# Kernel tuning notes

Hardware: AMD Instinct MI355X
Metric: run time of the kernel (lower is better)

Reference implementation:

```python
import jax, jax.numpy as jnp
import numpy as np

B, NA, LD, AD = 2048, 8, 256, 256
D = LD + AD            # token_dim = 512
E, K, H = 4, 2, 8      # n_experts, top_k, n_attention_heads
FFN, HEAD, BINS = 2048, 512, 101
DH = D // H
LN_EPS = 1e-5


def setup_inputs() -> dict:
    key = jax.random.key(0)
    ks = jax.random.split(key, 9)
    s = 0.02
    return {
        "latents": jax.random.normal(ks[0], (B, NA, LD), jnp.float32),
        "actions": jax.random.normal(ks[1], (B, NA, AD), jnp.float32),
        "gate_W": jax.random.normal(ks[2], (NA * D, E), jnp.float32) * s,
        "Wqkv": jax.random.normal(ks[3], (E, D, 3 * D), jnp.float32) * s,
        "bqkv": jnp.zeros((E, 3 * D), jnp.float32),
        "Wo": jax.random.normal(ks[4], (E, D, D), jnp.float32) * s,
        "bo": jnp.zeros((E, D), jnp.float32),
        "ln1_g": jnp.ones((E, D), jnp.float32),
        "ln1_b": jnp.zeros((E, D), jnp.float32),
        "Wf1": jax.random.normal(ks[5], (E, D, FFN), jnp.float32) * s,
        "bf1": jnp.zeros((E, FFN), jnp.float32),
        "Wf2": jax.random.normal(ks[6], (E, FFN, D), jnp.float32) * s,
        "bf2": jnp.zeros((E, D), jnp.float32),
        "ln2_g": jnp.ones((E, D), jnp.float32),
        "ln2_b": jnp.zeros((E, D), jnp.float32),
        "head_W1": jax.random.normal(ks[7], (NA * D, HEAD), jnp.float32) * s,
        "head_b1": jnp.zeros((HEAD,), jnp.float32),
        "head_W2": jax.random.normal(ks[8], (HEAD, BINS), jnp.float32) * s,
        "head_b2": jnp.zeros((BINS,), jnp.float32),
    }


def _layernorm(x, g, b):
    mu = x.mean(-1, keepdims=True)
    var = ((x - mu) ** 2).mean(-1, keepdims=True)
    return (x - mu) / jnp.sqrt(var + LN_EPS) * g + b


def _expert(tokens, Wqkv, bqkv, Wo, bo, g1, b1, Wf1, bf1, Wf2, bf2, g2, b2):
    # tokens: [B, N, D] -> self-attention + FFN block (pre-residual, post-LN)
    b, n, d = tokens.shape
    qkv = tokens @ Wqkv + bqkv                                  # [B, N, 3D]
    q, k, v = jnp.split(qkv, 3, axis=-1)
    heads = lambda x: x.reshape(b, n, H, DH).transpose(0, 2, 1, 3)  # [B, H, N, dh]
    q, k, v = heads(q), heads(k), heads(v)
    scores = jnp.einsum("bhqd,bhkd->bhqk", q, k) / np.float32(np.sqrt(DH))
    attn = jax.nn.softmax(scores, axis=-1)
    ctx = jnp.einsum("bhqk,bhkd->bhqd", attn, v).transpose(0, 2, 1, 3).reshape(b, n, d)
    x = _layernorm(tokens + ctx @ Wo + bo, g1, b1)
    h = jax.nn.relu(x @ Wf1 + bf1) @ Wf2 + bf2
    return _layernorm(x + h, g2, b2)


def _cv2(x):
    # coefficient of variation squared (unbiased var, matches torch .var())
    x = x.astype(jnp.float32)
    return jnp.var(x, ddof=1) / (jnp.mean(x) ** 2 + 1e-10)


def reference(latents, actions, gate_W, Wqkv, bqkv, Wo, bo, ln1_g, ln1_b,
              Wf1, bf1, Wf2, bf2, ln2_g, ln2_b, head_W1, head_b1, head_W2, head_b2):
    tokens = jnp.concatenate([latents, actions], axis=-1)       # [B, NA, D]
    flat = tokens.reshape(B, -1)
    # --- router (eval mode: clean logits, no noise) ---
    logits = flat @ gate_W                                      # [B, E]
    topv, topi = jax.lax.top_k(logits, min(K + 1, E))
    gk = jax.nn.softmax(topv[:, :K], axis=1)
    gates = jnp.zeros_like(logits).at[jnp.arange(B)[:, None], topi[:, :K]].set(gk)
    # --- experts: run all densely; zero-gate tokens contribute nothing,
    #     identical math to the original masked dispatch/combine ---
    expert_out = jax.vmap(_expert, in_axes=(None,) + (0,) * 12)(
        tokens, Wqkv, bqkv, Wo, bo, ln1_g, ln1_b, Wf1, bf1, Wf2, bf2, ln2_g, ln2_b)  # [E, B, N, D]
    mixed = jnp.einsum("be,ebnd->bnd", gates, expert_out)
    reward_logits = jax.nn.relu(mixed.reshape(B, -1) @ head_W1 + head_b1) @ head_W2 + head_b2
    # --- aux: load balancing loss ---
    load = (gates > 0).sum(0)
    lbl = _cv2(gates.sum(0)) + _cv2(load) + jnp.mean(jax.nn.logsumexp(logits, axis=-1))
    return reward_logits, gates, lbl
```

## Files before the change

kernel.cpp:

```cpp
#include <hip/hip_runtime.h>
#include <stdint.h>

#define NB    2048
#define NAG   8
#define NEXP  4
#define LN_EPS 1e-5f

#define OUT_GATES  (2048*101)
#define OUT_LBL    (OUT_GATES + 2048*4)

typedef __attribute__((ext_vector_type(8))) short short8;
typedef __attribute__((ext_vector_type(4))) float f32x4;

#define MFMA_BF16(a,b,c) __builtin_amdgcn_mfma_f32_16x16x32_bf16((a),(b),(c),0,0,0)

__device__ __forceinline__ float bf2f(unsigned short h){
  union { unsigned int u; float f; } v; v.u = ((unsigned int)h) << 16; return v.f;
}
__device__ __forceinline__ unsigned short f2bf(float x){
  union { float f; unsigned int u; } v; v.f = x;
  unsigned int r = v.u + 0x7FFFu + ((v.u >> 16) & 1u);
  return (unsigned short)(r >> 16);
}
union bfpack8 { short8 v; unsigned short u[8]; };

__device__ __forceinline__ void gload16(const void* g, void* l){
  __builtin_amdgcn_global_load_lds(
      (const __attribute__((address_space(1))) void*)g,
      (__attribute__((address_space(3))) void*)l, 16, 0, 0);
}

#define FBAR() do{ asm volatile("" ::: "memory"); \
                   __builtin_amdgcn_s_barrier(); \
                   asm volatile("" ::: "memory"); }while(0)

#define OFF_WQKVT  0ULL
#define OFF_WOT    6291456ULL
#define OFF_WF1T   8388608ULL
#define OFF_WF2T   16777216ULL
#define OFF_HW1T   25165824ULL
#define OFF_HW2T   29360128ULL
#define OFF_XBF    29474816ULL
#define OFF_SLOTO  63029248ULL
#define OFF_HID    96583680ULL
#define OFF_JOBS   98680832ULL
#define OFF_SLOTW  98713600ULL
#define OFF_LSE    98729984ULL
#define OFF_CNT    98738176ULL
#define WS_NEED    98738192ULL

__global__ __launch_bounds__(256) void k_transpose_cast(const float* __restrict__ src,
    unsigned short* __restrict__ dst, int R, int C){
  __shared__ float tile[32][33];
  int e = blockIdx.z;
  int c0 = blockIdx.x*32, r0 = blockIdx.y*32;
  const float* s = src + (size_t)e*R*C;
  unsigned short* d = dst + (size_t)e*C*R;
  int tx = threadIdx.x & 31, ty = threadIdx.x >> 5;
  for(int yy = ty; yy < 32; yy += 8){
    int r = r0+yy, c = c0+tx;
    if(r<R && c<C) tile[yy][tx] = s[(size_t)r*C + c];
  }
  __syncthreads();
  for(int yy = ty; yy < 32; yy += 8){
    int oc = c0+yy, orr = r0+tx;
    if(oc<C && orr<R) d[(size_t)oc*R + orr] = f2bf(tile[tx][yy]);
  }
}

__global__ __launch_bounds__(256) void k_router(const float* __restrict__ lat,
    const float* __restrict__ act, const float* __restrict__ gateW,
    float* __restrict__ gates_out, int* __restrict__ jobs, int* __restrict__ cnt,
    float* __restrict__ slot_w, float* __restrict__ lse_arr){
  int b = blockIdx.x, t = threadIdx.x;
  float a0=0.f,a1=0.f,a2=0.f,a3=0.f;
  for(int i=t;i<4096;i+=256){
    int n=i>>9, d=i&511;
    float v = (d<256)? lat[((size_t)b*8+n)*256 + d] : act[((size_t)b*8+n)*256 + (d-256)];
    float4 gw = *(const float4*)&gateW[(size_t)i*4];
    a0 += v*gw.x; a1 += v*gw.y; a2 += v*gw.z; a3 += v*gw.w;
  }
  __shared__ float red[4][256];
  red[0][t]=a0; red[1][t]=a1; red[2][t]=a2; red[3][t]=a3;
  __syncthreads();
  for(int s=128;s>0;s>>=1){
    if(t<s){ red[0][t]+=red[0][t+s]; red[1][t]+=red[1][t+s]; red[2][t]+=red[2][t+s]; red[3][t]+=red[3][t+s]; }
    __syncthreads();
  }
  if(t==0){
    float lg[4] = {red[0][0], red[1][0], red[2][0], red[3][0]};
    int i1=0; for(int e=1;e<4;e++) if(lg[e]>lg[i1]) i1=e;
    int i2=-1; for(int e=0;e<4;e++){ if(e==i1) continue; if(i2<0 || lg[e]>lg[i2]) i2=e; }
    float m = lg[i1];
    float e2 = __expf(lg[i2]-m);
    float inv = 1.f/(1.f+e2);
    float w1 = inv, w2 = e2*inv;
    float g[4]={0.f,0.f,0.f,0.f}; g[i1]=w1; g[i2]=w2;
    gates_out[b*4+0]=g[0]; gates_out[b*4+1]=g[1]; gates_out[b*4+2]=g[2]; gates_out[b*4+3]=g[3];
    float s=0.f; for(int e=0;e<4;e++) s += __expf(lg[e]-m);
    lse_arr[b] = m + __logf(s);
    int p1 = atomicAdd(&cnt[i1],1); jobs[i1*2048+p1] = b*2+0; slot_w[b*2+0] = w1;
    int p2 = atomicAdd(&cnt[i2],1); jobs[i2*2048+p2] = b*2+1; slot_w[b*2+1] = w2;
  }
}

__global__ __launch_bounds__(256) void k_finalize(const float* __restrict__ gates,
    const float* __restrict__ lse_arr, const int* __restrict__ cnt, float* __restrict__ lbl){
  __shared__ float r0[256], r1[256], r2[256], r3[256], rl[256];
  int t = threadIdx.x;
  float g0=0.f,g1=0.f,g2=0.f,g3=0.f,l=0.f;
  for(int b=t;b<2048;b+=256){
    g0+=gates[b*4+0]; g1+=gates[b*4+1]; g2+=gates[b*4+2]; g3+=gates[b*4+3];
    l += lse_arr[b];
  }
  r0[t]=g0;r1[t]=g1;r2[t]=g2;r3[t]=g3;rl[t]=l;
  __syncthreads();
  for(int s=128;s>0;s>>=1){
    if(t<s){ r0[t]+=r0[t+s]; r1[t]+=r1[t+s]; r2[t]+=r2[t+s]; r3[t]+=r3[t+s]; rl[t]+=rl[t+s]; }
    __syncthreads();
  }
  if(t==0){
    float gs[4]={r0[0],r1[0],r2[0],r3[0]};
    float ld[4]={(float)cnt[0],(float)cnt[1],(float)cnt[2],(float)cnt[3]};
    float mu1=(gs[0]+gs[1]+gs[2]+gs[3])*0.25f;
    float v1=0.f; for(int i=0;i<4;i++){float d=gs[i]-mu1; v1+=d*d;} v1 *= (1.f/3.f);
    float mu2=(ld[0]+ld[1]+ld[2]+ld[3])*0.25f;
    float v2=0.f; for(int i=0;i<4;i++){float d=ld[i]-mu2; v2+=d*d;} v2 *= (1.f/3.f);
    lbl[0] = v1/(mu1*mu1+1e-10f) + v2/(mu2*mu2+1e-10f) + rl[0]*(1.f/2048.f);
  }
}

#define AT_LDS 149504

#define STAGE_QKV(hh_, ks_, dst_) do{ \
    _Pragma("unroll") \
    for(int _q=0;_q<3;_q++){ \
      unsigned _L = (unsigned)w*3072u + (unsigned)_q*1024u + (unsigned)lane*16u; \
      int _row = (int)(_L>>7); unsigned _pb = _L & 127u; \
      int _gc = (_row<64)? (hh_)*64+_row : (_row<128)? 512+(hh_)*64+(_row-64) : 1024+(hh_)*64+(_row-128); \
      const char* _g = Wq + (size_t)_gc*1024 + (ks_)*128 + (_pb ^ ((unsigned)(_row&7)<<4)); \
      gload16(_g, (dst_) + ((unsigned)w*3072u + (unsigned)_q*1024u)); \
    } }while(0)

#define STAGE_WO(hg_, s_, dst_) do{ \
    int _nh = (s_)>>2, _k2 = (s_)&3; \
    _Pragma("unroll") \
    for(int _q=0;_q<2;_q++){ \
      unsigned _L = (unsigned)w*2048u + (unsigned)_q*1024u + (unsigned)lane*16u; \
      int _row = (int)(_L>>7); unsigned _pb = _L & 127u; \
      const char* _g = WoP + (size_t)(_nh*128+_row)*1024 + (hg_)*512 + _k2*128 \
                     + (_pb ^ ((unsigned)(_row&7)<<4)); \
      gload16(_g, (dst_) + ((unsigned)w*2048u + (unsigned)_q*1024u)); \
    } }while(0)

__global__ __launch_bounds__(512,2) void k_expert_attn(
    const float* __restrict__ lat, const float* __restrict__ act,
    const unsigned short* __restrict__ Wqkv_t, const float* __restrict__ bqkv,
    const unsigned short* __restrict__ Wo_t,   const float* __restrict__ bo,
    const float* __restrict__ ln1g, const float* __restrict__ ln1b,
    const int* __restrict__ jobs, const int* __restrict__ cnt,
    unsigned short* __restrict__ x_bf){
  extern __shared__ char smem[];
  char* Abase = smem;
  char* CTXb  = smem + 65536;
  char* U     = smem + 98304;
  float* SC   = (float*)(smem + 147456);

  int bid = blockIdx.x;
  int e   = (bid&7)>>1;
  int blk = ((bid>>3)<<1) | (bid&1);
  int ne = cnt[e];
  int base = blk*8;
  if(base >= ne) return;
  int t = threadIdx.x;
  int w = t>>6, lane = t&63, lg = lane>>4, lm = lane&15;
  int mt = w>>1, wb = w&1;
  const int* jb = &jobs[e*2048 + base];

  #pragma unroll
  for(int i=0;i<8;i++){
    int u = i*512 + t; int row = u>>6, ch = u&63; int d0 = ch*8;
    int j = row>>3;
    int slot = (base + j < ne) ? jb[j] : jb[0];
    int b = slot>>1, n = row&7;
    const float* src = (d0<256)? &lat[((size_t)b*8+n)*256 + d0]
                               : &act[((size_t)b*8+n)*256 + (d0-256)];
    float4 f0 = *(const float4*)src; float4 f1 = *(const float4*)(src+4);
    bfpack8 pk;
    pk.u[0]=f2bf(f0.x); pk.u[1]=f2bf(f0.y); pk.u[2]=f2bf(f0.z); pk.u[3]=f2bf(f0.w);
    pk.u[4]=f2bf(f1.x); pk.u[5]=f2bf(f1.y); pk.u[6]=f2bf(f1.z); pk.u[7]=f2bf(f1.w);
    *(short8*)(Abase + (((unsigned)(row*1024 + ch*16)) ^ ((unsigned)(row&7)<<4))) = pk.v;
  }
  asm volatile("s_waitcnt lgkmcnt(0)" ::: "memory");

  const char* Wq  = (const char*)(Wqkv_t + (size_t)e*1536*512);
  const char* WoP = (const char*)(Wo_t   + (size_t)e*512*512);
  unsigned short* QH = (unsigned short*)U;

  f32x4 acc2[4][4];
  #pragma unroll
  for(int a=0;a<4;a++)
    #pragma unroll
    for(int b2=0;b2<4;b2++) acc2[a][b2]=(f32x4){0.f,0.f,0.f,0.f};

  for(int hg=0; hg<2; hg++){
    for(int hh=0; hh<4; hh++){
      int h = hg*4 + hh;
      f32x4 acc1[6];
      #pragma unroll
      for(int i=0;i<6;i++) acc1[i]=(f32x4){0.f,0.f,0.f,0.f};

      STAGE_QKV(h, 0, U);
      #pragma unroll
      for(int ks=0; ks<8; ks++){
        char* nxt = U + (((ks+1)&1) ? 24576u : 0u);
        if(ks<7) STAGE_QKV(h, ks+1, nxt);
        if(ks<7) asm volatile("s_waitcnt vmcnt(3)" ::: "memory");
        else     asm volatile("s_waitcnt vmcnt(0)" ::: "memory");
        FBAR();
        const char* bs = U + ((ks&1) ? 24576u : 0u);
        int arow = mt*16+lm;
        #pragma unroll
        for(int half=0; half<2; half++){
          short8 a = *(const short8*)(Abase + (unsigned)arow*1024u
                       + (((unsigned)(ks*128 + half*64 + lg*16)) ^ ((unsigned)(arow&7)<<4)));
          #pragma unroll
          for(int i=0;i<6;i++){
            int brow = (wb*6+i)*16+lm;
            short8 bb = *(const short8*)(bs + (unsigned)brow*128u
                         + (((unsigned)(half*64+lg*16)) ^ ((unsigned)(brow&7)<<4)));
            acc1[i] = MFMA_BF16(a, bb, acc1[i]);
          }
        }
        FBAR();
      }
      #pragma unroll
      for(int i=0;i<6;i++){
        int L = (wb*6+i)*16 + lm;
        int gc = (L<64)? h*64+L : (L<128)? 512+h*64+(L-64) : 1024+h*64+(L-128);
        float bia = bqkv[e*1536 + gc];
        #pragma unroll
        for(int rr=0;rr<4;rr++){
          int row = mt*16 + lg*4 + rr;
          QH[row*200 + L] = f2bf(acc1[i][rr] + bia);
        }
      }
      __syncthreads();
      {
        int r = t>>3, p = t&7, j = r>>3;
        float s = 0.f;
        #pragma unroll
        for(int dd=0; dd<64; dd+=8){
          bfpack8 qa; qa.v = *(const short8*)&QH[r*200 + dd];
          bfpack8 ka; ka.v = *(const short8*)&QH[(j*8+p)*200 + 64 + dd];
          #pragma unroll
          for(int ii=0;ii<8;ii++) s += bf2f(qa.u[ii])*bf2f(ka.u[ii]);
        }
        SC[r*8+p] = s * 0.125f;
      }
      __syncthreads();
      {
        int r = t>>3, p = t&7, j = r>>3;
        float sv[8]; float m = -1e30f;
        #pragma unroll
        for(int kk=0;kk<8;kk++){ sv[kk]=SC[r*8+kk]; m = fmaxf(m, sv[kk]); }
        float ssum = 0.f;
        #pragma unroll
        for(int kk=0;kk<8;kk++){ sv[kk]=__expf(sv[kk]-m); ssum += sv[kk]; }
        float inv = 1.f/ssum;
        float o[8] = {0.f,0.f,0.f,0.f,0.f,0.f,0.f,0.f};
        #pragma unroll
        for(int kk=0;kk<8;kk++){
          float pr = sv[kk]*inv;
          bfpack8 va; va.v = *(const short8*)&QH[(j*8+kk)*200 + 128 + p*8];
          #pragma unroll
          for(int ii=0;ii<8;ii++) o[ii] += pr * bf2f(va.u[ii]);
        }
        bfpack8 pk;
        #pragma unroll
        for(int ii=0;ii<8;ii++) pk.u[ii]=f2bf(o[ii]);
        *(short8*)(CTXb + (((unsigned)(r*512 + hh*128 + p*16)) ^ ((unsigned)(r&7)<<4))) = pk.v;
      }
      __syncthreads();
    }

    STAGE_WO(hg, 0, U);
    #pragma unroll
    for(int s=0; s<16; s++){
      int nh = s>>2, k2 = s&3;
      char* nxt = U + (((s+1)&1) ? 16384u : 0u);
      if(s<15) STAGE_WO(hg, s+1, nxt);
      if(s<15) asm volatile("s_waitcnt vmcnt(2)" ::: "memory");
      else     asm volatile("s_waitcnt vmcnt(0)" ::: "memory");
      FBAR();
      const char* bs = U + ((s&1) ? 16384u : 0u);
      int arow = mt*16+lm;
      #pragma unroll
      for(int half=0; half<2; half++){
        short8 a = *(const short8*)(CTXb + (unsigned)arow*512u
                     + (((unsigned)(k2*128 + half*64 + lg*16)) ^ ((unsigned)(arow&7)<<4)));
        #pragma unroll
        for(int i=0;i<4;i++){
          int brow = (wb*4+i)*16+lm;
          short8 bb = *(const short8*)(bs + (unsigned)brow*128u
                       + (((unsigned)(half*64+lg*16)) ^ ((unsigned)(brow&7)<<4)));
          acc2[nh][i] = MFMA_BF16(a, bb, acc2[nh][i]);
        }
      }
      FBAR();
    }
  }

  #pragma unroll
  for(int nh=0; nh<4; nh++)
    #pragma unroll
    for(int i=0;i<4;i++){
      int gcol = nh*128 + (wb*4+i)*16 + lm;
      float bia = bo[e*512 + gcol];
      #pragma unroll
      for(int rr=0;rr<4;rr++){
        int row = mt*16 + lg*4 + rr;
        int j2 = row>>3;
        int slot = (base+j2<ne)? jb[j2] : jb[0];
        int b = slot>>1, n = row&7;
        float tok = (gcol<256)? lat[((size_t)b*8+n)*256 + gcol]
                              : act[((size_t)b*8+n)*256 + gcol - 256];
        *(unsigned short*)(Abase + (((unsigned)(row*1024 + gcol*2)) ^ ((unsigned)(row&7)<<4)))
            = f2bf(acc2[nh][i][rr] + bia + tok);
      }
    }
  __syncthreads();
  {
    int r = t>>3, p = t&7;
    unsigned rsw = ((unsigned)(r&7))<<4;
    bfpack8 xv[8];
    float sum=0.f, sq=0.f;
    #pragma unroll
    for(int j=0;j<8;j++){
      xv[j].v = *(const short8*)(Abase + (((unsigned)(r*1024 + j*128 + p*16)) ^ rsw));
      #pragma unroll
      for(int ii=0;ii<8;ii++){ float f = bf2f(xv[j].u[ii]); sum += f; sq += f*f; }
    }
    sum += __shfl_xor(sum,1); sq += __shfl_xor(sq,1);
    sum += __shfl_xor(sum,2); sq += __shfl_xor(sq,2);
    sum += __shfl_xor(sum,4); sq += __shfl_xor(sq,4);
    float mu = sum*(1.f/512.f);
    float var = sq*(1.f/512.f) - mu*mu;
    float rstd = rsqrtf(var + LN_EPS);
    int j8 = r>>3;
    if(base + j8 < ne){
      int slot = jb[j8]; int n = r&7;
      unsigned short* dst = &x_bf[((size_t)slot*8+n)*512];
      #pragma unroll
      for(int j=0;j<8;j++){
        bfpack8 pk;
        #pragma unroll
        for(int ii=0;ii<8;ii++){
          int gc = j*64 + p*8 + ii;
          float xvv = (bf2f(xv[j].u[ii]) - mu)*rstd*ln1g[e*512+gc] + ln1b[e*512+gc];
          pk.u[ii] = f2bf(xvv);
        }
        *(short8*)&dst[j*64 + p*8] = pk.v;
      }
    }
  }
}

#define E2_LDS 132096
#define E2_HP  264

#define FFN_STAGE_W1(cc, kk, dstoff) do{ \
    unsigned _Lw = (unsigned)w*4096u; \
    _Pragma("unroll") \
    for(int _q=0;_q<4;_q++){ \
      unsigned _L = _Lw + (unsigned)_q*1024u + (unsigned)lane*16u; \
      int _row = (int)(_L>>7); unsigned _pb = _L&127u; \
      const char* _g = W1 + (size_t)((cc)*256+_row)*1024 + (kk)*128 + (_pb ^ ((unsigned)(_row&7)<<4)); \
      gload16(_g, smem + (dstoff) + _Lw + (unsigned)_q*1024u); \
    } }while(0)

#define FFN_STAGE_W2(cc, nn, kk, dstoff) do{ \
    unsigned _Lw = (unsigned)w*4096u; \
    _Pragma("unroll") \
    for(int _q=0;_q<4;_q++){ \
      unsigned _L = _Lw + (unsigned)_q*1024u + (unsigned)lane*16u; \
      int _row = (int)(_L>>7); unsigned _pb = _L&127u; \
      const char* _g = W2 + (size_t)((nn)*256+_row)*4096 + ((cc)*256+(kk)*64)*2 \
                     + (_pb ^ ((unsigned)(_row&7)<<4)); \
      gload16(_g, smem + (dstoff) + _Lw + (unsigned)_q*1024u); \
    } }while(0)

#define ROT3() do{ unsigned _tmp=cur; cur=nxt; nxt=spr; spr=_tmp; }while(0)

__global__ __launch_bounds__(512,2) void k_expert_ffn(
    const unsigned short* __restrict__ x_bf,
    const unsigned short* __restrict__ Wf1_t, const float* __restrict__ bf1,
    const unsigned short* __restrict__ Wf2_t, const float* __restrict__ bf2v,
    const float* __restrict__ ln2g, const float* __restrict__ ln2b,
    const int* __restrict__ jobs, const int* __restrict__ cnt,
    unsigned short* __restrict__ slot_out){
  extern __shared__ char smem[];
  unsigned short* HC = (unsigned short*)(smem + 98304);
  unsigned short* PL = (unsigned short*)smem;

  int bid = blockIdx.x;
  int e   = (bid&7)>>1;
  int blk = ((bid>>3)<<1) | (bid&1);
  int ne = cnt[e];
  int base = blk*8;
  if(base >= ne) return;
  int t = threadIdx.x;
  int w = t>>6, lane = t&63, lg = lane>>4, lm = lane&15;
  int mg = w>>2, ng = w&3;
  const int* jb = &jobs[e*2048 + base];
  unsigned bswz = ((unsigned)(lm&7))<<4;

  const char* W1 = (const char*)(Wf1_t + (size_t)e*2048*512);
  const char* W2 = (const char*)(Wf2_t + (size_t)e*512*2048);

  const char* xb[2];
  #pragma unroll
  for(int ms=0;ms<2;ms++){
    int row = mg*32 + ms*16 + lm;
    int j = row>>3;
    int slot = (base+j<ne)? jb[j] : jb[0];
    int n = row&7;
    xb[ms] = (const char*)x_bf + (((size_t)slot*8+n)<<10) + (size_t)(lg*16);
  }

  short8 xf[2][2][2];
  #pragma unroll
  for(int ms=0;ms<2;ms++)
    #pragma unroll
    for(int hf=0;hf<2;hf++)
      xf[0][ms][hf] = *(const short8*)(xb[ms] + hf*64);

  f32x4 acc[2][2][4];
  #pragma unroll
  for(int a=0;a<2;a++)
    #pragma unroll
    for(int b=0;b<2;b++)
      #pragma unroll
      for(int c2=0;c2<4;c2++) acc[a][b][c2]=(f32x4){0.f,0.f,0.f,0.f};

  unsigned cur=0u, nxt=32768u, spr=65536u;

  FFN_STAGE_W1(0, 0, cur);

  for(int c=0; c<8; c++){
    f32x4 acc1[2][4];
    #pragma unroll
    for(int b=0;b<2;b++)
      #pragma unroll
      for(int c2=0;c2<4;c2++) acc1[b][c2]=(f32x4){0.f,0.f,0.f,0.f};

    #pragma unroll
    for(int ks=0; ks<8; ks++){
      #pragma unroll
      for(int ms=0;ms<2;ms++)
        #pragma unroll
        for(int hf=0;hf<2;hf++)
          xf[(ks+1)&1][ms][hf] = *(const short8*)(xb[ms] + (((ks+1)&7)*128 + hf*64));
      if(ks<7) FFN_STAGE_W1(c, ks+1, nxt);
      else     FFN_STAGE_W2(c, 0, 0, nxt);
      asm volatile("s_waitcnt vmcnt(8)" ::: "memory");
      FBAR();
      const char* bs = smem + cur;
      #pragma unroll
      for(int hf=0;hf<2;hf++){
        #pragma unroll
        for(int ns=0;ns<4;ns++){
          unsigned boff = (unsigned)(((ng*4+ns)*16+lm)*128);
          short8 bb = *(const short8*)(bs + boff + (((unsigned)(hf*64+lg*16)) ^ bswz));
          acc1[0][ns] = MFMA_BF16(xf[ks&1][0][hf], bb, acc1[0][ns]);
          acc1[1][ns] = MFMA_BF16(xf[ks&1][1][hf], bb, acc1[1][ns]);
        }
      }
      if(ks==7){
        #pragma unroll
        for(int ms=0;ms<2;ms++)
          #pragma unroll
          for(int ns=0;ns<4;ns++){
            int colL = ng*64 + ns*16 + lm;
            float bia = bf1[e*2048 + c*256 + colL];
            #pragma unroll
            for(int rr=0;rr<4;rr++){
              int row = mg*32 + ms*16 + lg*4 + rr;
              HC[row*E2_HP + colL] = f2bf(fmaxf(acc1[ms][ns][rr] + bia, 0.f));
            }
          }
        asm volatile("s_waitcnt lgkmcnt(0)" ::: "memory");
      }
      ROT3();
    }

    #pragma unroll
    for(int s2=0; s2<8; s2++){
      const int nh = s2>>2, k2 = s2&3;
      if(s2<7)      FFN_STAGE_W2(c, (s2+1)>>2, (s2+1)&3, nxt);
      else if(c<7)  FFN_STAGE_W1(c+1, 0, nxt);
      if(s2==7 && c==7) asm volatile("s_waitcnt vmcnt(0)" ::: "memory");
      else              asm volatile("s_waitcnt vmcnt(4)" ::: "memory");
      FBAR();
      const char* bs = smem + cur;
      #pragma unroll
      for(int hf=0;hf<2;hf++){
        short8 ha0 = *(const short8*)&HC[(mg*32 +      lm)*E2_HP + k2*64 + hf*32 + lg*8];
        short8 ha1 = *(const short8*)&HC[(mg*32 + 16 + lm)*E2_HP + k2*64 + hf*32 + lg*8];
        #pragma unroll
        for(int ns=0;ns<4;ns++){
          unsigned boff = (unsigned)(((ng*4+ns)*16+lm)*128);
          short8 bb = *(const short8*)(bs + boff + (((unsigned)(hf*64+lg*16)) ^ bswz));
          acc[nh][0][ns] = MFMA_BF16(ha0, bb, acc[nh][0][ns]);
          acc[nh][1][ns] = MFMA_BF16(ha1, bb, acc[nh][1][ns]);
        }
      }
      ROT3();
    }
  }
  __syncthreads();

  #pragma unroll
  for(int nh=0;nh<2;nh++)
    #pragma unroll
    for(int ms=0;ms<2;ms++)
      #pragma unroll
      for(int ns=0;ns<4;ns++){
        int col = nh*256 + ng*64 + ns*16 + lm;
        float bia = bf2v[e*512+col];
        #pragma unroll
        for(int rr=0;rr<4;rr++){
          int row = mg*32 + ms*16 + lg*4 + rr;
          PL[row*520 + col] = f2bf(acc[nh][ms][ns][rr] + bia);
        }
      }
  __syncthreads();

  {
    int r = t>>3, p = t&7;
    int j8 = r>>3;
    int slot = (base + j8 < ne) ? jb[j8] : jb[0];
    int n = r&7;
    const unsigned short* xg = &x_bf[((size_t)slot*8+n)*512];
    bfpack8 cv[8];
    float sum=0.f, sq=0.f;
    #pragma unroll
    for(int j=0;j<8;j++){
      bfpack8 pa; pa.v = *(const short8*)&PL[r*520 + j*64 + p*8];
      bfpack8 xa; xa.v = *(const short8*)&xg[j*64 + p*8];
      #pragma unroll
      for(int ii=0;ii<8;ii++){
        float f = bf2f(pa.u[ii]) + bf2f(xa.u[ii]);
        cv[j].u[ii] = f2bf(f);
        f = bf2f(cv[j].u[ii]);
        sum += f; sq += f*f;
      }
    }
    sum += __shfl_xor(sum,1); sq += __shfl_xor(sq,1);
    sum += __shfl_xor(sum,2); sq += __shfl_xor(sq,2);
    sum += __shfl_xor(sum,4); sq += __shfl_xor(sq,4);
    float mu = sum*(1.f/512.f);
    float var = sq*(1.f/512.f) - mu*mu;
    float rstd = rsqrtf(var + LN_EPS);
    if(base + j8 < ne){
      unsigned short* dst = &slot_out[((size_t)slot*8+n)*512];
      #pragma unroll
      for(int j=0;j<8;j++){
        bfpack8 pk;
        #pragma unroll
        for(int ii=0;ii<8;ii++){
          int gc = j*64 + p*8 + ii;
          float xv = (bf2f(cv[j].u[ii]) - mu)*rstd*ln2g[e*512+gc] + ln2b[e*512+gc];
          pk.u[ii] = f2bf(xv);
        }
        *(short8*)&dst[j*64 + p*8] = pk.v;
      }
    }
  }
}

__global__ __launch_bounds__(256) void k_combine(const unsigned short* __restrict__ so,
    const float* __restrict__ slotw, unsigned short* __restrict__ mx){
  int gid = blockIdx.x*256 + threadIdx.x;
  int b = gid >> 9, c8 = gid & 511;
  float w0 = slotw[b*2+0], w1 = slotw[b*2+1];
  bfpack8 x0; x0.v = *(const short8*)&so[((size_t)(b*2+0))*4096 + c8*8];
  bfpack8 x1; x1.v = *(const short8*)&so[((size_t)(b*2+1))*4096 + c8*8];
  bfpack8 o;
  #pragma unroll
  for(int j=0;j<8;j++) o.u[j] = f2bf(w0*bf2f(x0.u[j]) + w1*bf2f(x1.u[j]));
  *(short8*)&mx[(size_t)b*4096 + c8*8] = o.v;
}

#define H_SP 72
__global__ __launch_bounds__(256) void k_head1(const unsigned short* __restrict__ mixbf,
    const unsigned short* __restrict__ hW1t, const float* __restrict__ b1,
    unsigned short* __restrict__ hidden){
  __shared__ unsigned short As[64*H_SP], Bs[64*H_SP];
  int n0 = blockIdx.x*64, m0 = blockIdx.y*64;
  int t = threadIdx.x, w = t>>6, lane = t&63, lg = lane>>4, lm = lane&15;
  f32x4 acc[4]; for(int i=0;i<4;i++) acc[i]=(f32x4){0.f,0.f,0.f,0.f};
  for(int ks=0; ks<64; ks++){
    __syncthreads();
    int k0 = ks*64;
    for(int i=0;i<2;i++){
      int u = i*256 + t; int row = u>>3, ch = u&7;
      *(short8*)&As[row*H_SP + ch*8] = *(const short8*)&mixbf[(size_t)(m0+row)*4096 + k0 + ch*8];
    }
    for(int i=0;i<2;i++){
      int u = i*256 + t; int row = u>>3, ch = u&7;
      *(short8*)&Bs[row*H_SP + ch*8] = *(const short8*)&hW1t[(size_t)(n0+row)*4096 + k0 + ch*8];
    }
    __syncthreads();
    for(int half=0; half<2; half++){
      short8 a = *(const short8*)&As[(w*16+lm)*H_SP + half*32 + lg*8];
      for(int i=0;i<4;i++){
        short8 bb = *(const short8*)&Bs[(i*16+lm)*H_SP + half*32 + lg*8];
        acc[i] = MFMA_BF16(a, bb, acc[i]);
      }
    }
  }
  for(int i=0;i<4;i++){
    int gc = n0 + i*16 + lm; float bia = b1[gc];
    for(int rr=0; rr<4; rr++){
      int row = m0 + w*16 + lg*4 + rr;
      hidden[(size_t)row*512 + gc] = f2bf(fmaxf(acc[i][rr] + bia, 0.f));
    }
  }
}

__global__ __launch_bounds__(256) void k_head2(const unsigned short* __restrict__ hidden,
    const unsigned short* __restrict__ hW2t, const float* __restrict__ b2,
    float* __restrict__ out){
  __shared__ unsigned short As[64*H_SP], Bs[112*H_SP];
  int m0 = blockIdx.x*64;
  int t = threadIdx.x, w = t>>6, lane = t&63, lg = lane>>4, lm = lane&15;
  f32x4 acc[7]; for(int i=0;i<7;i++) acc[i]=(f32x4){0.f,0.f,0.f,0.f};
  for(int ks=0; ks<8; ks++){
    __syncthreads();
    int k0 = ks*64;
    for(int i=0;i<2;i++){
      int u = i*256 + t; int row = u>>3, ch = u&7;
      *(short8*)&As[row*H_SP + ch*8] = *(const short8*)&hidden[(size_t)(m0+row)*512 + k0 + ch*8];
    }
    for(int i=0;i<4;i++){
      int u = i*256 + t;
      if(u < 896){
        int row = u>>3, ch = u&7;
        *(short8*)&Bs[row*H_SP + ch*8] = *(const short8*)&hW2t[(size_t)row*512 + k0 + ch*8];
      }
    }
    __syncthreads();
    for(int half=0; half<2; half++){
      short8 a = *(const short8*)&As[(w*16+lm)*H_SP + half*32 + lg*8];
      for(int i=0;i<7;i++){
        short8 bb = *(const short8*)&Bs[(i*16+lm)*H_SP + half*32 + lg*8];
        acc[i] = MFMA_BF16(a, bb, acc[i]);
      }
    }
  }
  for(int i=0;i<7;i++){
    int col = i*16 + lm;
    if(col < 101){
      float bia = b2[col];
      for(int rr=0; rr<4; rr++){
        int row = m0 + w*16 + lg*4 + rr;
        out[(size_t)row*101 + col] = acc[i][rr] + bia;
      }
    }
  }
}

extern "C" void kernel_launch(void* const* d_in, const int* in_sizes, int n_in,
                              void* d_out, int out_size, void* d_ws, size_t ws_size,
                              hipStream_t stream){
  if(ws_size < WS_NEED) return;
  const float* lat  = (const float*)d_in[0];
  const float* act  = (const float*)d_in[1];
  const float* gateW= (const float*)d_in[2];
  const float* Wqkv = (const float*)d_in[3];
  const float* bqkv = (const float*)d_in[4];
  const float* Wo   = (const float*)d_in[5];
  const float* bo   = (const float*)d_in[6];
  const float* ln1g = (const float*)d_in[7];
  const float* ln1b = (const float*)d_in[8];
  const float* Wf1  = (const float*)d_in[9];
  const float* bf1  = (const float*)d_in[10];
  const float* Wf2  = (const float*)d_in[11];
  const float* bf2v = (const float*)d_in[12];
  const float* ln2g = (const float*)d_in[13];
  const float* ln2b = (const float*)d_in[14];
  const float* hW1  = (const float*)d_in[15];
  const float* hb1  = (const float*)d_in[16];
  const float* hW2  = (const float*)d_in[17];
  const float* hb2  = (const float*)d_in[18];
  float* out = (float*)d_out;
  char* ws = (char*)d_ws;

  unsigned short* WQKVT = (unsigned short*)(ws + OFF_WQKVT);
  unsigned short* WOT   = (unsigned short*)(ws + OFF_WOT);
  unsigned short* WF1T  = (unsigned short*)(ws + OFF_WF1T);
  unsigned short* WF2T  = (unsigned short*)(ws + OFF_WF2T);
  unsigned short* HW1T  = (unsigned short*)(ws + OFF_HW1T);
  unsigned short* HW2T  = (unsigned short*)(ws + OFF_HW2T);
  unsigned short* XBF   = (unsigned short*)(ws + OFF_XBF);
  unsigned short* SLOTO = (unsigned short*)(ws + OFF_SLOTO);
  unsigned short* MIXBF = XBF;
  unsigned short* HID = (unsigned short*)(ws + OFF_HID);
  int* JOBS = (int*)(ws + OFF_JOBS);
  float* SLOTW = (float*)(ws + OFF_SLOTW);
  float* LSE = (float*)(ws + OFF_LSE);
  int* CNT = (int*)(ws + OFF_CNT);

  (void)hipFuncSetAttribute((const void*)k_expert_attn,
      hipFuncAttributeMaxDynamicSharedMemorySize, AT_LDS);
  (void)hipFuncSetAttribute((const void*)k_expert_ffn,
      hipFuncAttributeMaxDynamicSharedMemorySize, E2_LDS);

  hipMemsetAsync(CNT, 0, 16, stream);
  hipMemsetAsync(HW2T, 0, 112*512*2, stream);

  k_transpose_cast<<<dim3(48,16,4),256,0,stream>>>(Wqkv, WQKVT, 512, 1536);
  k_transpose_cast<<<dim3(16,16,4),256,0,stream>>>(Wo,   WOT,   512, 512);
  k_transpose_cast<<<dim3(64,16,4),256,0,stream>>>(Wf1,  WF1T,  512, 2048);
  k_transpose_cast<<<dim3(16,64,4),256,0,stream>>>(Wf2,  WF2T,  2048, 512);
  k_transpose_cast<<<dim3(16,128,1),256,0,stream>>>(hW1, HW1T,  4096, 512);
  k_transpose_cast<<<dim3(4,16,1),256,0,stream>>>(hW2,  HW2T,  512, 101);

  k_router<<<2048,256,0,stream>>>(lat, act, gateW, out + OUT_GATES, JOBS, CNT, SLOTW, LSE);
  k_finalize<<<1,256,0,stream>>>(out + OUT_GATES, LSE, CNT, out + OUT_LBL);

  k_expert_attn<<<1024, 512, AT_LDS, stream>>>(lat, act, WQKVT, bqkv, WOT, bo,
      ln1g, ln1b, JOBS, CNT, XBF);
  k_expert_ffn<<<1024, 512, E2_LDS, stream>>>(XBF, WF1T, bf1, WF2T, bf2v,
      ln2g, ln2b, JOBS, CNT, SLOTO);
  k_combine<<<4096,256,0,stream>>>(SLOTO, SLOTW, MIXBF);

  k_head1<<<dim3(8,32),256,0,stream>>>(MIXBF, HW1T, hb1, HID);
  k_head2<<<32,256,0,stream>>>(HID, HW2T, hb2, out);
}
```

Baseline: 780.7 us.

## Process two attention heads per QKV GEMM pass with 2x-M warp tiling

The QKV projection loop now computes two heads at once (384 output columns), using 16 smaller k-steps instead of 8 per head. Each warp covers 32 rows by 96 columns, so every B fragment feeds two MFMAs. The QH buffer is widened to hold both heads, and the score and softmax stages loop over the pair. This halves the number of outer passes and their barriers and improves B-fragment reuse, at the cost of more accumulator registers and a larger LDS footprint, which could reduce occupancy.

```diff
diff --git a/kernel.cpp b/kernel.cpp
--- a/kernel.cpp
+++ b/kernel.cpp
@@ -130,15 +130,19 @@
   }
 }
 
-#define AT_LDS 149504
-
-#define STAGE_QKV(hh_, ks_, dst_) do{ \
+#define AT_LDS 153600
+
+#define STAGE_QKV2(hp_, ks_, dst_) do{ \
     _Pragma("unroll") \
     for(int _q=0;_q<3;_q++){ \
       unsigned _L = (unsigned)w*3072u + (unsigned)_q*1024u + (unsigned)lane*16u; \
-      int _row = (int)(_L>>7); unsigned _pb = _L & 127u; \
-      int _gc = (_row<64)? (hh_)*64+_row : (_row<128)? 512+(hh_)*64+(_row-64) : 1024+(hh_)*64+(_row-128); \
-      const char* _g = Wq + (size_t)_gc*1024 + (ks_)*128 + (_pb ^ ((unsigned)(_row&7)<<4)); \
+      unsigned _line = _L>>7; unsigned _wb7 = _L & 127u; \
+      unsigned _un = _wb7 ^ ((_line&7u)<<4); \
+      int _row = (int)(_line*2u + (_un>>6)); \
+      unsigned _kb = _un & 63u; \
+      int _hsel = (_row>=192); int _rr = _row - 192*_hsel; \
+      int _seg = _rr>>6; int _gc = _seg*512 + ((hp_)*2+_hsel)*64 + (_rr&63); \
+      const char* _g = Wq + (size_t)_gc*1024 + (size_t)((ks_)*64) + _kb; \
       gload16(_g, (dst_) + ((unsigned)w*3072u + (unsigned)_q*1024u)); \
     } }while(0)
 
@@ -164,7 +168,7 @@
   char* Abase = smem;
   char* CTXb  = smem + 65536;
   char* U     = smem + 98304;
-  float* SC   = (float*)(smem + 147456);
+  float* SCp  = (float*)(smem + 149504);
 
   int bid = blockIdx.x;
   int e   = (bid&7)>>1;
@@ -175,6 +179,7 @@
   int t = threadIdx.x;
   int w = t>>6, lane = t&63, lg = lane>>4, lm = lane&15;
   int mt = w>>1, wb = w&1;
+  int mg = w>>2, ng = w&3;
   const int* jb = &jobs[e*2048 + base];
 
   #pragma unroll
@@ -204,82 +209,99 @@
     for(int b2=0;b2<4;b2++) acc2[a][b2]=(f32x4){0.f,0.f,0.f,0.f};
 
   for(int hg=0; hg<2; hg++){
-    for(int hh=0; hh<4; hh++){
-      int h = hg*4 + hh;
-      f32x4 acc1[6];
-      #pragma unroll
-      for(int i=0;i<6;i++) acc1[i]=(f32x4){0.f,0.f,0.f,0.f};
-
-      STAGE_QKV(h, 0, U);
-      #pragma unroll
-      for(int ks=0; ks<8; ks++){
+    for(int hpl=0; hpl<2; hpl++){
+      int hp = hg*2 + hpl;
+      f32x4 acc1[2][6];
+      #pragma unroll
+      for(int m2=0;m2<2;m2++)
+        #pragma unroll
+        for(int i=0;i<6;i++) acc1[m2][i]=(f32x4){0.f,0.f,0.f,0.f};
+
+      STAGE_QKV2(hp, 0, U);
+      #pragma unroll
+      for(int ks=0; ks<16; ks++){
         char* nxt = U + (((ks+1)&1) ? 24576u : 0u);
-        if(ks<7) STAGE_QKV(h, ks+1, nxt);
-        if(ks<7) asm volatile("s_waitcnt vmcnt(3)" ::: "memory");
-        else     asm volatile("s_waitcnt vmcnt(0)" ::: "memory");
+        if(ks<15) STAGE_QKV2(hp, ks+1, nxt);
+        if(ks<15) asm volatile("s_waitcnt vmcnt(3)" ::: "memory");
+        else      asm volatile("s_waitcnt vmcnt(0)" ::: "memory");
         FBAR();
         const char* bs = U + ((ks&1) ? 24576u : 0u);
-        int arow = mt*16+lm;
-        #pragma unroll
-        for(int half=0; half<2; half++){
-          short8 a = *(const short8*)(Abase + (unsigned)arow*1024u
-                       + (((unsigned)(ks*128 + half*64 + lg*16)) ^ ((unsigned)(arow&7)<<4)));
+        int r0 = mg*32 + lm, r1 = r0 + 16;
+        short8 a0 = *(const short8*)(Abase + (unsigned)r0*1024u
+                     + (((unsigned)(ks*64 + lg*16)) ^ ((unsigned)(r0&7)<<4)));
+        short8 a1 = *(const short8*)(Abase + (unsigned)r1*1024u
+                     + (((unsigned)(ks*64 + lg*16)) ^ ((unsigned)(r1&7)<<4)));
+        #pragma unroll
+        for(int i=0;i<6;i++){
+          int brow = (ng*6+i)*16 + lm;
+          unsigned bline = (unsigned)(brow>>1);
+          unsigned bo = bline*128u
+                      + ((((unsigned)(brow&1))<<6 | ((unsigned)lg<<4)) ^ ((bline&7u)<<4));
+          short8 bb = *(const short8*)(bs + bo);
+          acc1[0][i] = MFMA_BF16(a0, bb, acc1[0][i]);
+          acc1[1][i] = MFMA_BF16(a1, bb, acc1[1][i]);
+        }
+        FBAR();
+      }
+      #pragma unroll
+      for(int m2=0;m2<2;m2++)
+        #pragma unroll
+        for(int i=0;i<6;i++){
+          int L = (ng*6+i)*16 + lm;
+          int hsel = (L>=192); int LL = L - 192*hsel;
+          int seg = LL>>6; int c6 = LL&63;
+          int gc = seg*512 + (hp*2+hsel)*64 + c6;
+          float bia = bqkv[e*1536 + gc];
           #pragma unroll
-          for(int i=0;i<6;i++){
-            int brow = (wb*6+i)*16+lm;
-            short8 bb = *(const short8*)(bs + (unsigned)brow*128u
-                         + (((unsigned)(half*64+lg*16)) ^ ((unsigned)(brow&7)<<4)));
-            acc1[i] = MFMA_BF16(a, bb, acc1[i]);
+          for(int rr=0;rr<4;rr++){
+            int row = mg*32 + m2*16 + lg*4 + rr;
+            QH[row*400 + hsel*200 + seg*64 + c6] = f2bf(acc1[m2][i][rr] + bia);
           }
         }
-        FBAR();
-      }
-      #pragma unroll
-      for(int i=0;i<6;i++){
-        int L = (wb*6+i)*16 + lm;
-        int gc = (L<64)? h*64+L : (L<128)? 512+h*64+(L-64) : 1024+h*64+(L-128);
-        float bia = bqkv[e*1536 + gc];
-        #pragma unroll
-        for(int rr=0;rr<4;rr++){
-          int row = mt*16 + lg*4 + rr;
-          QH[row*200 + L] = f2bf(acc1[i][rr] + bia);
-        }
-      }
       __syncthreads();
       {
         int r = t>>3, p = t&7, j = r>>3;
-        float s = 0.f;
-        #pragma unroll
-        for(int dd=0; dd<64; dd+=8){
-          bfpack8 qa; qa.v = *(const short8*)&QH[r*200 + dd];
-          bfpack8 ka; ka.v = *(const short8*)&QH[(j*8+p)*200 + 64 + dd];
+        #pragma unroll
+        for(int hsel=0; hsel<2; hsel++){
+          const unsigned short* qrow = &QH[r*400 + hsel*200];
+          const unsigned short* krow = &QH[(j*8+p)*400 + hsel*200 + 64];
+          float s = 0.f;
           #pragma unroll
-          for(int ii=0;ii<8;ii++) s += bf2f(qa.u[ii])*bf2f(ka.u[ii]);
-        }
-        SC[r*8+p] = s * 0.125f;
+          for(int dd=0; dd<64; dd+=8){
+            bfpack8 qa; qa.v = *(const short8*)&qrow[dd];
+            bfpack8 ka; ka.v = *(const short8*)&krow[dd];
+            #pragma unroll
+            for(int ii=0;ii<8;ii++) s += bf2f(qa.u[ii])*bf2f(ka.u[ii]);
+          }
+          SCp[hsel*512 + r*8 + p] = s * 0.125f;
+        }
       }
       __syncthreads();
       {
         int r = t>>3, p = t&7, j = r>>3;
-        float sv[8]; float m = -1e30f;
-        #pragma unroll
-        for(int kk=0;kk<8;kk++){ sv[kk]=SC[r*8+kk]; m = fmaxf(m, sv[kk]); }
-        float ssum = 0.f;
-        #pragma unroll
-        for(int kk=0;kk<8;kk++){ sv[kk]=__expf(sv[kk]-m); ssum += sv[kk]; }
-        float inv = 1.f/ssum;
-        float o[8] = {0.f,0.f,0.f,0.f,0.f,0.f,0.f,0.f};
-        #pragma unroll
-        for(int kk=0;kk<8;kk++){
-          float pr = sv[kk]*inv;
-          bfpack8 va; va.v = *(const short8*)&QH[(j*8+kk)*200 + 128 + p*8];
+        #pragma unroll
+        for(int hsel=0; hsel<2; hsel++){
+          float sv[8]; float m = -1e30f;
           #pragma unroll
-          for(int ii=0;ii<8;ii++) o[ii] += pr * bf2f(va.u[ii]);
-        }
-        bfpack8 pk;
-        #pragma unroll
-        for(int ii=0;ii<8;ii++) pk.u[ii]=f2bf(o[ii]);
-        *(short8*)(CTXb + (((unsigned)(r*512 + hh*128 + p*16)) ^ ((unsigned)(r&7)<<4))) = pk.v;
+          for(int kk=0;kk<8;kk++){ sv[kk]=SCp[hsel*512 + r*8 + kk]; m = fmaxf(m, sv[kk]); }
+          float ssum = 0.f;
+          #pragma unroll
+          for(int kk=0;kk<8;kk++){ sv[kk]=__expf(sv[kk]-m); ssum += sv[kk]; }
+          float inv = 1.f/ssum;
+          float o[8] = {0.f,0.f,0.f,0.f,0.f,0.f,0.f,0.f};
+          #pragma unroll
+          for(int kk=0;kk<8;kk++){
+            float pr = sv[kk]*inv;
+            bfpack8 va; va.v = *(const short8*)&QH[(j*8+kk)*400 + hsel*200 + 128 + p*8];
+            #pragma unroll
+            for(int ii=0;ii<8;ii++) o[ii] += pr * bf2f(va.u[ii]);
+          }
+          bfpack8 pk;
+          #pragma unroll
+          for(int ii=0;ii<8;ii++) pk.u[ii]=f2bf(o[ii]);
+          int lh = (hp*2+hsel)&3;
+          *(short8*)(CTXb + (((unsigned)(r*512 + lh*128 + p*16)) ^ ((unsigned)(r&7)<<4))) = pk.v;
+        }
       }
       __syncthreads();
     }
```

After: 785.7 us. About the same (+0.6%).
